# Performance work log

Measured on AMD Instinct MI355X. Metric: run time of the kernel, lower is better.

The kernel has to match this reference:

```python
import jax, jax.numpy as jnp
import numpy as np

B, S, T, C, HS = 32, 8, 512, 128, 128


def setup_inputs() -> dict:
    key = jax.random.key(0)
    k1, k2, k3, k4, k5 = jax.random.split(key, 5)
    x = jax.random.normal(k1, (B, T, C), dtype=jnp.float32)
    adjacent = jax.random.uniform(k2, (B, S, T, T), dtype=jnp.float32)
    scale = 1.0 / np.sqrt(C)
    Wq = jax.random.normal(k3, (C, HS), dtype=jnp.float32) * scale
    Wk = jax.random.normal(k4, (C, HS), dtype=jnp.float32) * scale
    Wv = jax.random.normal(k5, (C, HS), dtype=jnp.float32) * scale
    return {"x": x, "adjacent": adjacent, "Wq": Wq, "Wk": Wk, "Wv": Wv}


def reference(x, adjacent, Wq, Wk, Wv):
    # x: [B,T,C], adjacent: [B,S,T,T]
    Cdim = x.shape[-1]
    q = x @ Wq            # [B,T,HS]
    k = x @ Wk            # [B,T,HS]
    v = x @ Wv            # [B,T,HS]
    # scaled scores (note: original scales by C^-0.5, not head_size^-0.5)
    wei = jnp.einsum('btd,bud->btu', q, k) * (Cdim ** -0.5)  # [B,T,T]
    # multiplicative adjacency mask, broadcast over S
    wei = wei[:, None, :, :] * adjacent                       # [B,S,T,T]
    wei = jax.nn.softmax(wei, axis=-1)
    # dropout p=0.0 -> identity
    out = jnp.einsum('bstu,bud->bstd', wei, v)                # [B,S,T,HS]
    return out
```

## Files before the change

kernel.cpp:

```cpp
#include <hip/hip_runtime.h>
#include <hip/hip_bf16.h>
#include <stdint.h>

#define NB 32
#define NS 8
#define NT 512
#define NC 128
#define NH 128

typedef __bf16 bf16_t;
typedef bf16_t bf16x8 __attribute__((ext_vector_type(8)));
typedef bf16_t bf16x4 __attribute__((ext_vector_type(4)));
typedef float  f32x4  __attribute__((ext_vector_type(4)));

__global__ __launch_bounds__(256) void k_split(const float* __restrict__ in,
                                               bf16_t* __restrict__ hi,
                                               bf16_t* __restrict__ lo, int n4) {
  int i = blockIdx.x * 256 + threadIdx.x;
  if (i >= n4) return;
  f32x4 x = ((const f32x4*)in)[i];
  bf16x4 h, l;
#pragma unroll
  for (int j = 0; j < 4; j++) {
    bf16_t hb = (bf16_t)x[j];
    h[j] = hb;
    l[j] = (bf16_t)(x[j] - (float)hb);
  }
  ((bf16x4*)hi)[i] = h;
  ((bf16x4*)lo)[i] = l;
}

__global__ void k_prep_w(const float* __restrict__ Wq, const float* __restrict__ Wk,
                         const float* __restrict__ Wv, bf16_t* __restrict__ Wth,
                         bf16_t* __restrict__ Wtl) {
  int w = blockIdx.x >> 7;
  int h = blockIdx.x & 127;
  int c = threadIdx.x;
  const float* W = (w == 0) ? Wq : (w == 1) ? Wk : Wv;
  float x = W[c * NH + h];
  if (w == 0) x *= 0.08838834764831845f;
  bf16_t hb = (bf16_t)x;
  int o = (w * 128 + h) * 128 + c;
  Wth[o] = hb;
  Wtl[o] = (bf16_t)(x - (float)hb);
}

__global__ __launch_bounds__(256) void k_qkv(const bf16_t* __restrict__ xh,
                                             const bf16_t* __restrict__ xl,
                                             const bf16_t* __restrict__ Wth,
                                             const bf16_t* __restrict__ Wtl,
                                             bf16_t* __restrict__ qh,
                                             bf16_t* __restrict__ ql,
                                             bf16_t* __restrict__ kh,
                                             bf16_t* __restrict__ kl,
                                             bf16_t* __restrict__ vt) {
  int mat = blockIdx.y;
  int t0 = blockIdx.x * 64;
  int lane = threadIdx.x & 63;
  int wave = threadIdx.x >> 6;
  int l15 = lane & 15;
  int kq = (lane >> 4) * 8;
  int row = t0 + wave * 16 + l15;
  const bf16_t* Wh = Wth + mat * NC * NH;
  const bf16_t* Wl = Wtl + mat * NC * NH;

  f32x4 zero = {0.f, 0.f, 0.f, 0.f};
  f32x4 acc[8];
#pragma unroll
  for (int i = 0; i < 8; i++) acc[i] = zero;

#pragma unroll
  for (int k0 = 0; k0 < NC; k0 += 32) {
    bf16x8 ah = *(const bf16x8*)(xh + (size_t)row * NC + k0 + kq);
    bf16x8 al = *(const bf16x8*)(xl + (size_t)row * NC + k0 + kq);
#pragma unroll
    for (int nt = 0; nt < 8; nt++) {
      bf16x8 bh = *(const bf16x8*)(Wh + (nt * 16 + l15) * NC + k0 + kq);
      bf16x8 bl = *(const bf16x8*)(Wl + (nt * 16 + l15) * NC + k0 + kq);
      acc[nt] = __builtin_amdgcn_mfma_f32_16x16x32_bf16(ah, bh, acc[nt], 0, 0, 0);
      acc[nt] = __builtin_amdgcn_mfma_f32_16x16x32_bf16(ah, bl, acc[nt], 0, 0, 0);
      acc[nt] = __builtin_amdgcn_mfma_f32_16x16x32_bf16(al, bh, acc[nt], 0, 0, 0);
    }
  }

  int trow = t0 + wave * 16 + (lane >> 4) * 4;
  if (mat < 2) {
    bf16_t* dh = (mat == 0) ? qh : kh;
    bf16_t* dl = (mat == 0) ? ql : kl;
#pragma unroll
    for (int nt = 0; nt < 8; nt++) {
      int h = nt * 16 + l15;
#pragma unroll
      for (int r = 0; r < 4; r++) {
        float v = acc[nt][r];
        bf16_t hb = (bf16_t)v;
        dh[(size_t)(trow + r) * NH + h] = hb;
        dl[(size_t)(trow + r) * NH + h] = (bf16_t)(v - (float)hb);
      }
    }
  } else {
    int b = trow >> 9;
    int tl = trow & 511;
#pragma unroll
    for (int nt = 0; nt < 8; nt++) {
      int h = nt * 16 + l15;
      bf16x4 pk;
#pragma unroll
      for (int r = 0; r < 4; r++) pk[r] = (bf16_t)acc[nt][r];
      *(bf16x4*)(vt + ((size_t)b * NH + h) * NT + tl) = pk;
    }
  }
}

#define PLD 520

__global__ __launch_bounds__(512, 8) void k_attn(const bf16_t* __restrict__ qh,
                                                 const bf16_t* __restrict__ ql,
                                                 const bf16_t* __restrict__ kh,
                                                 const bf16_t* __restrict__ kl,
                                                 const float* __restrict__ adj,
                                                 const bf16_t* __restrict__ vt,
                                                 float* __restrict__ out) {
  __shared__ bf16_t p[2][16 * PLD];
  int t0 = blockIdx.x * 16;
  int b = blockIdx.y;
  int lane = threadIdx.x & 63;
  int wave = threadIdx.x >> 6;
  int l15 = lane & 15;
  int q4 = lane >> 4;
  int kq = q4 * 8;
  int u0 = wave * 64;
  int h0 = wave * 16;

  f32x4 zero = {0.f, 0.f, 0.f, 0.f};
  f32x4 wacc[4];
#pragma unroll
  for (int i = 0; i < 4; i++) wacc[i] = zero;
  {
    size_t qb = ((size_t)b * NT + t0 + l15) * NH;
    size_t kb = ((size_t)b * NT + u0 + l15) * NH;
#pragma unroll
    for (int k0 = 0; k0 < NH; k0 += 32) {
      bf16x8 ah = *(const bf16x8*)(qh + qb + k0 + kq);
      bf16x8 al = *(const bf16x8*)(ql + qb + k0 + kq);
#pragma unroll
      for (int nt = 0; nt < 4; nt++) {
        bf16x8 bh = *(const bf16x8*)(kh + kb + (size_t)nt * 16 * NH + k0 + kq);
        bf16x8 bl = *(const bf16x8*)(kl + kb + (size_t)nt * 16 * NH + k0 + kq);
        wacc[nt] = __builtin_amdgcn_mfma_f32_16x16x32_bf16(ah, bh, wacc[nt], 0, 0, 0);
        wacc[nt] = __builtin_amdgcn_mfma_f32_16x16x32_bf16(ah, bl, wacc[nt], 0, 0, 0);
        wacc[nt] = __builtin_amdgcn_mfma_f32_16x16x32_bf16(al, bh, wacc[nt], 0, 0, 0);
      }
    }
  }

  const bf16_t* vb = vt + (size_t)b * NH * NT;
  bf16x8 ones;
#pragma unroll
  for (int j = 0; j < 8; j++) ones[j] = (bf16_t)1.0f;

  for (int s = 0; s < NS; s++) {
    bf16_t* pb = &p[s & 1][0];
    const float* abase =
        adj + (((size_t)b * NS + s) * NT + t0 + q4 * 4) * NT + u0 + l15;
#pragma unroll
    for (int nt = 0; nt < 4; nt++) {
#pragma unroll
      for (int r = 0; r < 4; r++) {
        float a = abase[(size_t)r * NT + nt * 16];
        float e = __expf(wacc[nt][r] * a);
        pb[(q4 * 4 + r) * PLD + u0 + nt * 16 + l15] = (bf16_t)e;
      }
    }
    __syncthreads();

    f32x4 acc = zero, accl = zero;
#pragma unroll 4
    for (int k0 = 0; k0 < NT; k0 += 32) {
      bf16x8 afr = *(const bf16x8*)&pb[l15 * PLD + k0 + kq];
      accl = __builtin_amdgcn_mfma_f32_16x16x32_bf16(afr, ones, accl, 0, 0, 0);
      bf16x8 bfr = *(const bf16x8*)(vb + (size_t)(h0 + l15) * NT + k0 + kq);
      acc = __builtin_amdgcn_mfma_f32_16x16x32_bf16(afr, bfr, acc, 0, 0, 0);
    }

    float* obase = out + (((size_t)b * NS + s) * NT + t0) * NH;
#pragma unroll
    for (int r = 0; r < 4; r++) {
      float linv = 1.0f / accl[r];
      obase[(size_t)(q4 * 4 + r) * NH + h0 + l15] = acc[r] * linv;
    }
  }
}

extern "C" void kernel_launch(void* const* d_in, const int* in_sizes, int n_in,
                              void* d_out, int out_size, void* d_ws, size_t ws_size,
                              hipStream_t stream) {
  const float* x = (const float*)d_in[0];
  const float* adj = (const float*)d_in[1];
  const float* Wq = (const float*)d_in[2];
  const float* Wk = (const float*)d_in[3];
  const float* Wv = (const float*)d_in[4];
  float* out = (float*)d_out;

  const size_t BTC = (size_t)NB * NT * NC;

  char* base = (char*)d_ws;
  bf16_t* xh = (bf16_t*)base;  base += BTC * 2;
  bf16_t* xl = (bf16_t*)base;  base += BTC * 2;
  bf16_t* Wth = (bf16_t*)base; base += (size_t)3 * NC * NH * 2;
  bf16_t* Wtl = (bf16_t*)base; base += (size_t)3 * NC * NH * 2;
  bf16_t* qh = (bf16_t*)base;  base += BTC * 2;
  bf16_t* ql = (bf16_t*)base;  base += BTC * 2;
  bf16_t* kh = (bf16_t*)base;  base += BTC * 2;
  bf16_t* kl = (bf16_t*)base;  base += BTC * 2;
  bf16_t* vt = (bf16_t*)base;  base += BTC * 2;
  (void)in_sizes; (void)n_in; (void)out_size; (void)ws_size;

  k_split<<<(int)(BTC / 4 / 256), 256, 0, stream>>>(x, xh, xl, (int)(BTC / 4));
  k_prep_w<<<384, 128, 0, stream>>>(Wq, Wk, Wv, Wth, Wtl);
  k_qkv<<<dim3((int)(NB * NT / 64), 3), 256, 0, stream>>>(xh, xl, Wth, Wtl,
                                                          qh, ql, kh, kl, vt);
  k_attn<<<dim3(NT / 16, NB), 512, 0, stream>>>(qh, ql, kh, kl, adj, vt, out);
}
```

Baseline: 537.1 us.

## Prefetch adjacency tiles into LDS asynchronously and keep V fragments in registers

The attention kernel now streams each step's adjacency tile straight from global memory into shared memory with global_load_lds. It issues the load for step s+1 while step s runs the PV MFMA, which overlaps the dominant adjacency read with compute. The V^T fragments are loaded once into registers instead of being re-read from global memory every step. The P buffer drops from double to single buffering, guarded by two barriers per step. Occupancy hints drop from 8 to 4 blocks, raising register pressure and adding the risk of synchronization mistakes.

```diff
diff --git a/kernel.cpp b/kernel.cpp
--- a/kernel.cpp
+++ b/kernel.cpp
@@ -12,6 +12,11 @@
 typedef bf16_t bf16x8 __attribute__((ext_vector_type(8)));
 typedef bf16_t bf16x4 __attribute__((ext_vector_type(4)));
 typedef float  f32x4  __attribute__((ext_vector_type(4)));
+
+#define GLOAD_LDS4(gp, lp)                                             \
+  __builtin_amdgcn_global_load_lds(                                    \
+      (const __attribute__((address_space(1))) uint32_t*)(gp),         \
+      (__attribute__((address_space(3))) uint32_t*)(lp), 4, 0, 0)
 
 __global__ __launch_bounds__(256) void k_split(const float* __restrict__ in,
                                                bf16_t* __restrict__ hi,
@@ -113,15 +118,17 @@
 }
 
 #define PLD 520
-
-__global__ __launch_bounds__(512, 8) void k_attn(const bf16_t* __restrict__ qh,
+#define ALD 66
+
+__global__ __launch_bounds__(512, 4) void k_attn(const bf16_t* __restrict__ qh,
                                                  const bf16_t* __restrict__ ql,
                                                  const bf16_t* __restrict__ kh,
                                                  const bf16_t* __restrict__ kl,
                                                  const float* __restrict__ adj,
                                                  const bf16_t* __restrict__ vt,
                                                  float* __restrict__ out) {
-  __shared__ bf16_t p[2][16 * PLD];
+  __shared__ bf16_t pbuf[16 * PLD];
+  __shared__ float adj_lds[8 * 16 * ALD];
   int t0 = blockIdx.x * 16;
   int b = blockIdx.y;
   int lane = threadIdx.x & 63;
@@ -131,6 +138,20 @@
   int kq = q4 * 8;
   int u0 = wave * 64;
   int h0 = wave * 16;
+  float* amy = &adj_lds[wave * 16 * ALD];
+
+  {
+    const float* src = adj + ((size_t)b * NS * NT + t0) * NT + u0;
+#pragma unroll
+    for (int row = 0; row < 16; row++)
+      GLOAD_LDS4(src + (size_t)row * NT + lane, amy + row * ALD);
+  }
+
+  const bf16_t* vb = vt + (size_t)b * NH * NT;
+  bf16x8 vtf[16];
+#pragma unroll
+  for (int k = 0; k < 16; k++)
+    vtf[k] = *(const bf16x8*)(vb + (size_t)(h0 + l15) * NT + k * 32 + kq);
 
   f32x4 zero = {0.f, 0.f, 0.f, 0.f};
   f32x4 wacc[4];
@@ -154,41 +175,49 @@
     }
   }
 
-  const bf16_t* vb = vt + (size_t)b * NH * NT;
   bf16x8 ones;
 #pragma unroll
   for (int j = 0; j < 8; j++) ones[j] = (bf16_t)1.0f;
 
+#pragma unroll 1
   for (int s = 0; s < NS; s++) {
-    bf16_t* pb = &p[s & 1][0];
-    const float* abase =
-        adj + (((size_t)b * NS + s) * NT + t0 + q4 * 4) * NT + u0 + l15;
-#pragma unroll
-    for (int nt = 0; nt < 4; nt++) {
+    asm volatile("s_waitcnt vmcnt(0)" ::: "memory");
+    __builtin_amdgcn_sched_barrier(0);
+
+#pragma unroll
+    for (int nt = 0; nt < 4; nt++)
 #pragma unroll
       for (int r = 0; r < 4; r++) {
-        float a = abase[(size_t)r * NT + nt * 16];
+        float a = amy[(q4 * 4 + r) * ALD + nt * 16 + l15];
         float e = __expf(wacc[nt][r] * a);
-        pb[(q4 * 4 + r) * PLD + u0 + nt * 16 + l15] = (bf16_t)e;
+        pbuf[(q4 * 4 + r) * PLD + u0 + nt * 16 + l15] = (bf16_t)e;
       }
-    }
-    __syncthreads();
+
+    asm volatile("s_waitcnt lgkmcnt(0)" ::: "memory");
+    __builtin_amdgcn_sched_barrier(0);
+    if (s + 1 < NS) {
+      const float* src = adj + (((size_t)b * NS + s + 1) * NT + t0) * NT + u0;
+#pragma unroll
+      for (int row = 0; row < 16; row++)
+        GLOAD_LDS4(src + (size_t)row * NT + lane, amy + row * ALD);
+    }
+
+    __builtin_amdgcn_s_barrier();
 
     f32x4 acc = zero, accl = zero;
-#pragma unroll 4
-    for (int k0 = 0; k0 < NT; k0 += 32) {
-      bf16x8 afr = *(const bf16x8*)&pb[l15 * PLD + k0 + kq];
+#pragma unroll
+    for (int k = 0; k < 16; k++) {
+      bf16x8 afr = *(const bf16x8*)&pbuf[l15 * PLD + k * 32 + kq];
       accl = __builtin_amdgcn_mfma_f32_16x16x32_bf16(afr, ones, accl, 0, 0, 0);
-      bf16x8 bfr = *(const bf16x8*)(vb + (size_t)(h0 + l15) * NT + k0 + kq);
-      acc = __builtin_amdgcn_mfma_f32_16x16x32_bf16(afr, bfr, acc, 0, 0, 0);
-    }
-
-    float* obase = out + (((size_t)b * NS + s) * NT + t0) * NH;
-#pragma unroll
-    for (int r = 0; r < 4; r++) {
-      float linv = 1.0f / accl[r];
-      obase[(size_t)(q4 * 4 + r) * NH + h0 + l15] = acc[r] * linv;
-    }
+      acc = __builtin_amdgcn_mfma_f32_16x16x32_bf16(afr, vtf[k], acc, 0, 0, 0);
+    }
+
+    float* obase = out + (((size_t)b * NS + s) * NT + t0 + q4 * 4) * NH;
+#pragma unroll
+    for (int r = 0; r < 4; r++)
+      obase[(size_t)r * NH + h0 + l15] = acc[r] * (1.0f / accl[r]);
+
+    __builtin_amdgcn_s_barrier();
   }
 }
 
```

Result: faster. 442.2 us (-17.7%).
